# Kernel tuning notes

Measured on AMD Instinct MI355X. Metric: run time of the kernel, lower is better.

## Reference

```python
import jax, jax.numpy as jnp
import numpy as np

N, IN_DIM, LDIM = 8192, 512, 256
NEG_SLOPE = 0.01  # torch F.leaky_relu default
EPS = 1e-10


def setup_inputs() -> dict:
    key = jax.random.key(0)
    k1, k2, k3, k4 = jax.random.split(key, 4)
    x = jax.random.normal(k1, (N, IN_DIM), dtype=jnp.float32)
    adj = jax.random.uniform(k2, (N, N), dtype=jnp.float32)
    # nn.Linear(in_dim, learning_dim, bias=False) weight: [learning_dim, in_dim]
    proj_w = jax.random.normal(k3, (LDIM, IN_DIM), dtype=jnp.float32) * (1.0 / np.sqrt(IN_DIM))
    # nn.init.uniform_(learn_w, a=0, b=1)
    learn_w = jax.random.uniform(k4, (LDIM,), dtype=jnp.float32)
    return {"x": x, "adj": adj, "proj_w": proj_w, "learn_w": learn_w}


def reference(x, adj, proj_w, learn_w):
    # x_hat = projection(x): [N, LDIM]
    x_hat = x @ proj_w.T
    # cosine-distance score: sum_d w_d * (1 - xn_i[d] * xn_j[d])
    #   = sum(w) - (xn * w) @ xn.T  -- avoids the N x N x D intermediate
    xn = x_hat / jnp.linalg.norm(x_hat, axis=-1, keepdims=True)  # [N, LDIM]
    scores = jnp.sum(learn_w) - jnp.einsum('id,jd->ij', xn * learn_w, xn)  # [N, N]
    out = jax.nn.leaky_relu(scores, NEG_SLOPE)
    out = out - jnp.max(out, axis=-1, keepdims=True)
    soft_adj = adj * jnp.exp(out)
    soft_adj = soft_adj / jnp.sum(soft_adj, axis=-1, keepdims=True) + EPS
    return soft_adj
```

## Files before the change

kernel.cpp:

```cpp
#include <hip/hip_runtime.h>
#include <stdint.h>

#define NN 8192
#define KDIM 512
#define LDIM 256

typedef short bf16x8 __attribute__((ext_vector_type(8)));
typedef short short8 __attribute__((ext_vector_type(8)));
typedef float f32x4 __attribute__((ext_vector_type(4)));

__device__ __forceinline__ unsigned short f2bf(float f) {
  unsigned int u = __float_as_uint(f);
  u = (u + 0x7fffu + ((u >> 16) & 1u)) >> 16;
  return (unsigned short)u;
}
__device__ __forceinline__ float bf2f(unsigned short s) {
  return __uint_as_float(((unsigned int)s) << 16);
}

__device__ __forceinline__ void async_ld16(const unsigned short* g, unsigned short* l) {
  __builtin_amdgcn_global_load_lds(
      (const __attribute__((address_space(1))) unsigned int*)g,
      (__attribute__((address_space(3))) unsigned int*)l, 16, 0, 0);
}

__global__ __launch_bounds__(256) void cast_kernel(
    const float* __restrict__ x, const float* __restrict__ pw,
    unsigned short* __restrict__ xb, unsigned short* __restrict__ pwb) {
  int i = blockIdx.x * 256 + threadIdx.x;
  xb[i] = f2bf(x[i]);
  if (i < LDIM * KDIM) pwb[i] = f2bf(pw[i]);
}

__global__ __launch_bounds__(256) void norm_kernel(
    const float* __restrict__ xh, const float* __restrict__ w,
    unsigned short* __restrict__ Ab, unsigned short* __restrict__ Bb) {
  const int row = blockIdx.x;
  const int d = threadIdx.x;
  const float v = xh[row * LDIM + d];
  float ss = v * v;
#pragma unroll
  for (int m = 1; m < 64; m <<= 1) ss += __shfl_xor(ss, m);
  __shared__ float s4[4];
  if ((d & 63) == 0) s4[d >> 6] = ss;
  __syncthreads();
  const float tot = s4[0] + s4[1] + s4[2] + s4[3];
  const float inv = 1.0f / sqrtf(tot);
  const float xn = v * inv;
  Bb[row * LDIM + d] = f2bf(xn);
  Ab[row * LDIM + d] = f2bf(xn * w[d]);
}

template <int K, int MODE>
__global__ __launch_bounds__(256) void gemm_bt(
    const unsigned short* __restrict__ A,
    const unsigned short* __restrict__ B,
    float* __restrict__ C,
    unsigned short* __restrict__ T,
    const float* __restrict__ adj,
    float* __restrict__ rowsum,
    int ldC) {
  __shared__ unsigned short As[128 * 32];
  __shared__ unsigned short Bs[128 * 32];
  __shared__ float rs[128];

  const int tid = threadIdx.x;
  const int wave = tid >> 6;
  const int lane = tid & 63;
  const int quad = lane >> 4;
  const int l16 = lane & 15;
  const int wm = wave >> 1;
  const int wn = wave & 1;

  const size_t row0 = (size_t)blockIdx.y * 128;
  const size_t col0 = (size_t)blockIdx.x * 128;

  const int c0 = wave * 128 + lane;
  const int mA = c0 >> 2;
  const int kA = (c0 & 3) * 8;
  const unsigned short* Ag = A + (row0 + mA) * (size_t)K + kA;
  const unsigned short* Bg = B + (col0 + mA) * (size_t)K + kA;
  char* AsB = (char*)As;
  char* BsB = (char*)Bs;
  unsigned short* dA0 = (unsigned short*)(AsB + wave * 2048);
  unsigned short* dA1 = (unsigned short*)(AsB + wave * 2048 + 1024);
  unsigned short* dB0 = (unsigned short*)(BsB + wave * 2048);
  unsigned short* dB1 = (unsigned short*)(BsB + wave * 2048 + 1024);

  f32x4 acc[4][4];
#pragma unroll
  for (int i = 0; i < 4; ++i)
#pragma unroll
    for (int j = 0; j < 4; ++j) acc[i][j] = (f32x4)(0.0f);

  for (int k0 = 0; k0 < K; k0 += 32) {
    async_ld16(Ag + k0, dA0);
    async_ld16(Ag + 16 * (size_t)K + k0, dA1);
    async_ld16(Bg + k0, dB0);
    async_ld16(Bg + 16 * (size_t)K + k0, dB1);
    __syncthreads();

    bf16x8 av[4], bv[4];
#pragma unroll
    for (int mt = 0; mt < 4; ++mt)
      av[mt] = *(const bf16x8*)(AsB + (wm * 64 + mt * 16 + l16) * 64 + quad * 16);
#pragma unroll
    for (int nt = 0; nt < 4; ++nt)
      bv[nt] = *(const bf16x8*)(BsB + (wn * 64 + nt * 16 + l16) * 64 + quad * 16);
#pragma unroll
    for (int mt = 0; mt < 4; ++mt)
#pragma unroll
      for (int nt = 0; nt < 4; ++nt)
        acc[mt][nt] = __builtin_amdgcn_mfma_f32_16x16x32_bf16(av[mt], bv[nt], acc[mt][nt], 0, 0, 0);
    __syncthreads();
  }

  if constexpr (MODE == 0) {
#pragma unroll
    for (int mt = 0; mt < 4; ++mt)
#pragma unroll
      for (int nt = 0; nt < 4; ++nt)
#pragma unroll
        for (int r = 0; r < 4; ++r) {
          size_t gr = row0 + wm * 64 + mt * 16 + quad * 4 + r;
          size_t gc = col0 + wn * 64 + nt * 16 + l16;
          C[gr * (size_t)ldC + gc] = acc[mt][nt][r];
        }
  } else {
    __shared__ float trans[32 * 132];
    const int s = tid >> 3;
    const int cb = tid & 7;
    const int coff = cb * 16;
#pragma unroll
    for (int mt = 0; mt < 4; ++mt) {
      __syncthreads();
#pragma unroll
      for (int nt = 0; nt < 4; ++nt)
#pragma unroll
        for (int r = 0; r < 4; ++r)
          trans[(wm * 16 + quad * 4 + r) * 132 + wn * 64 + nt * 16 + l16] =
              acc[mt][nt][r];
      __syncthreads();
      const size_t gr = row0 + (size_t)(s >> 4) * 64 + mt * 16 + (s & 15);
      const float* arow = adj + gr * NN + col0 + coff;
      float av16[16];
#pragma unroll
      for (int q = 0; q < 4; ++q) {
        float4 a4 = ((const float4*)arow)[q];
        av16[q * 4 + 0] = a4.x;
        av16[q * 4 + 1] = a4.y;
        av16[q * 4 + 2] = a4.z;
        av16[q * 4 + 3] = a4.w;
      }
      const float* drow = &trans[s * 132 + coff];
      float part = 0.0f;
      if constexpr (MODE == 1) {
        short8 p0, p1;
#pragma unroll
        for (int j = 0; j < 16; ++j) {
          float tv = av16[j] * __expf(-drow[j]);
          unsigned short us = f2bf(tv);
          part += bf2f(us);
          if (j < 8) p0[j] = (short)us; else p1[j - 8] = (short)us;
        }
        short8* trow = (short8*)(T + gr * NN + col0 + coff);
        trow[0] = p0;
        trow[1] = p1;
      } else {
        float4 o[4];
#pragma unroll
        for (int j = 0; j < 16; ++j) {
          float tv = av16[j] * __expf(-drow[j]);
          part += tv;
          ((float*)o)[j] = tv;
        }
        float4* crow = (float4*)(C + gr * NN + col0 + coff);
#pragma unroll
        for (int q = 0; q < 4; ++q) crow[q] = o[q];
      }
      part += __shfl_xor(part, 1);
      part += __shfl_xor(part, 2);
      part += __shfl_xor(part, 4);
      if (cb == 0) rs[(s >> 4) * 64 + mt * 16 + (s & 15)] = part;
    }
    __syncthreads();
    if (tid < 128) atomicAdd(&rowsum[row0 + tid], rs[tid]);
  }
}

__global__ __launch_bounds__(256) void scale_bf16_kernel(
    const unsigned short* __restrict__ T, const float* __restrict__ rowsum,
    float* __restrict__ out) {
  const size_t i = (size_t)blockIdx.x * 256 + threadIdx.x;
  const int row = (int)(i >> 10);
  short8 tv = ((const short8*)T)[i];
  const float inv = 1.0f / rowsum[row];
  float4 o0, o1;
  o0.x = bf2f((unsigned short)tv[0]) * inv + 1e-10f;
  o0.y = bf2f((unsigned short)tv[1]) * inv + 1e-10f;
  o0.z = bf2f((unsigned short)tv[2]) * inv + 1e-10f;
  o0.w = bf2f((unsigned short)tv[3]) * inv + 1e-10f;
  o1.x = bf2f((unsigned short)tv[4]) * inv + 1e-10f;
  o1.y = bf2f((unsigned short)tv[5]) * inv + 1e-10f;
  o1.z = bf2f((unsigned short)tv[6]) * inv + 1e-10f;
  o1.w = bf2f((unsigned short)tv[7]) * inv + 1e-10f;
  ((float4*)out)[i * 2] = o0;
  ((float4*)out)[i * 2 + 1] = o1;
}

__global__ __launch_bounds__(256) void scale_f32_kernel(
    float* __restrict__ t, const float* __restrict__ rowsum) {
  const size_t i = (size_t)blockIdx.x * 256 + threadIdx.x;
  const int row = (int)(i >> 11);
  float4 v = ((float4*)t)[i];
  const float inv = 1.0f / rowsum[row];
  v.x = v.x * inv + 1e-10f;
  v.y = v.y * inv + 1e-10f;
  v.z = v.z * inv + 1e-10f;
  v.w = v.w * inv + 1e-10f;
  ((float4*)t)[i] = v;
}

extern "C" void kernel_launch(void* const* d_in, const int* in_sizes, int n_in,
                              void* d_out, int out_size, void* d_ws, size_t ws_size,
                              hipStream_t stream) {
  (void)in_sizes; (void)n_in; (void)out_size;
  const float* x   = (const float*)d_in[0];
  const float* adj = (const float*)d_in[1];
  const float* pw  = (const float*)d_in[2];
  const float* lw  = (const float*)d_in[3];
  float* out = (float*)d_out;
  char* ws = (char*)d_ws;

  unsigned short* xb   = (unsigned short*)(ws);
  unsigned short* pwb  = (unsigned short*)(ws + 8388608);
  float*          xhat = (float*)(ws + 8650752);
  unsigned short* Ab   = (unsigned short*)(ws + 17039360);
  unsigned short* Bb   = (unsigned short*)(ws + 21233664);
  float*          rsum = (float*)(ws + 25427968);
  unsigned short* Tbuf = (unsigned short*)(ws + 25460736);
  const bool big_ws = ws_size >= 25460736ull + (size_t)NN * NN * 2ull;

  cast_kernel<<<(NN * KDIM) / 256, 256, 0, stream>>>(x, pw, xb, pwb);
  gemm_bt<KDIM, 0><<<dim3(2, 64), 256, 0, stream>>>(xb, pwb, xhat, nullptr, nullptr, nullptr, LDIM);
  norm_kernel<<<NN, 256, 0, stream>>>(xhat, lw, Ab, Bb);
  hipMemsetAsync(rsum, 0, NN * sizeof(float), stream);
  if (big_ws) {
    gemm_bt<LDIM, 1><<<dim3(64, 64), 256, 0, stream>>>(Ab, Bb, nullptr, Tbuf, adj, rsum, NN);
    scale_bf16_kernel<<<(NN / 8) * (NN / 256), 256, 0, stream>>>(Tbuf, rsum, out);
  } else {
    gemm_bt<LDIM, 2><<<dim3(64, 64), 256, 0, stream>>>(Ab, Bb, out, nullptr, adj, rsum, NN);
    scale_f32_kernel<<<(NN / 4) * (NN / 256), 256, 0, stream>>>(out, rsum);
  }
}
```

Baseline: 542.9 us.

## Fuse projection GEMM with row normalization, vectorize cast, swizzle score GEMM blocks

Replaces the projection GEMM plus separate norm kernel with one kernel. Each block computes a 32-row slab across all 256 output columns, reduces the row norms from the accumulators, and writes the normalized bf16 A/B operands directly, so the fp32 x_hat round trip and one launch go away. The cast kernel now handles four elements per thread with float4 loads. The big score GEMM remaps block indices with a swizzle, meant to improve L2 reuse of the A/B tiles. The large score GEMM and its adj/output traffic still dominate, so the overall effect may be small.

```diff
diff --git a/kernel.cpp b/kernel.cpp
--- a/kernel.cpp
+++ b/kernel.cpp
@@ -8,6 +8,7 @@
 typedef short bf16x8 __attribute__((ext_vector_type(8)));
 typedef short short8 __attribute__((ext_vector_type(8)));
 typedef float f32x4 __attribute__((ext_vector_type(4)));
+typedef unsigned short u16x4 __attribute__((ext_vector_type(4)));
 
 __device__ __forceinline__ unsigned short f2bf(float f) {
   unsigned int u = __float_as_uint(f);
@@ -18,7 +19,7 @@
   return __uint_as_float(((unsigned int)s) << 16);
 }
 
-__device__ __forceinline__ void async_ld16(const unsigned short* g, unsigned short* l) {
+__device__ __forceinline__ void async_ld16(const unsigned short* g, void* l) {
   __builtin_amdgcn_global_load_lds(
       (const __attribute__((address_space(1))) unsigned int*)g,
       (__attribute__((address_space(3))) unsigned int*)l, 16, 0, 0);
@@ -27,28 +28,125 @@
 __global__ __launch_bounds__(256) void cast_kernel(
     const float* __restrict__ x, const float* __restrict__ pw,
     unsigned short* __restrict__ xb, unsigned short* __restrict__ pwb) {
-  int i = blockIdx.x * 256 + threadIdx.x;
-  xb[i] = f2bf(x[i]);
-  if (i < LDIM * KDIM) pwb[i] = f2bf(pw[i]);
-}
-
-__global__ __launch_bounds__(256) void norm_kernel(
-    const float* __restrict__ xh, const float* __restrict__ w,
+  const int i = blockIdx.x * 256 + threadIdx.x;
+  float4 v = ((const float4*)x)[i];
+  u16x4 o;
+  o[0] = (short)f2bf(v.x); o[1] = (short)f2bf(v.y);
+  o[2] = (short)f2bf(v.z); o[3] = (short)f2bf(v.w);
+  ((u16x4*)xb)[i] = o;
+  if (i < (LDIM * KDIM) / 4) {
+    float4 w = ((const float4*)pw)[i];
+    u16x4 ow;
+    ow[0] = (short)f2bf(w.x); ow[1] = (short)f2bf(w.y);
+    ow[2] = (short)f2bf(w.z); ow[3] = (short)f2bf(w.w);
+    ((u16x4*)pwb)[i] = ow;
+  }
+}
+
+__global__ __launch_bounds__(256) void gemm1_norm_kernel(
+    const unsigned short* __restrict__ xb,
+    const unsigned short* __restrict__ pwb,
+    const float* __restrict__ w,
     unsigned short* __restrict__ Ab, unsigned short* __restrict__ Bb) {
-  const int row = blockIdx.x;
-  const int d = threadIdx.x;
-  const float v = xh[row * LDIM + d];
-  float ss = v * v;
-#pragma unroll
-  for (int m = 1; m < 64; m <<= 1) ss += __shfl_xor(ss, m);
-  __shared__ float s4[4];
-  if ((d & 63) == 0) s4[d >> 6] = ss;
+  __shared__ alignas(16) unsigned short As[32 * 32];
+  __shared__ alignas(16) unsigned short Bs[256 * 32];
+  __shared__ float nrm[32][5];
+  __shared__ float wS[LDIM];
+  __shared__ alignas(16) unsigned short xnS[32][264];
+  __shared__ alignas(16) unsigned short anS[32][264];
+
+  const int tid = threadIdx.x;
+  const int wave = tid >> 6;
+  const int lane = tid & 63;
+  const int quad = lane >> 4;
+  const int l16 = lane & 15;
+  const size_t row0 = (size_t)blockIdx.x * 32;
+
+  if (tid < LDIM) wS[tid] = w[tid];
+
+  f32x4 acc[2][4];
+#pragma unroll
+  for (int i = 0; i < 2; ++i)
+#pragma unroll
+    for (int j = 0; j < 4; ++j) acc[i][j] = (f32x4)(0.0f);
+
+  for (int k0 = 0; k0 < KDIM; k0 += 32) {
+#pragma unroll
+    for (int j = 0; j < 4; ++j) {
+      const int c = (wave * 4 + j) * 64 + lane;
+      async_ld16(pwb + (size_t)(c >> 2) * KDIM + (c & 3) * 8 + k0,
+                 (char*)Bs + (wave * 4 + j) * 1024);
+    }
+    if (wave == 0) {
+#pragma unroll
+      for (int j2 = 0; j2 < 2; ++j2) {
+        const int c = j2 * 64 + lane;
+        async_ld16(xb + (row0 + (c >> 2)) * (size_t)KDIM + (c & 3) * 8 + k0,
+                   (char*)As + j2 * 1024);
+      }
+    }
+    __syncthreads();
+    bf16x8 av[2], bv[4];
+#pragma unroll
+    for (int mt = 0; mt < 2; ++mt)
+      av[mt] = *(const bf16x8*)(As + (mt * 16 + l16) * 32 + quad * 8);
+#pragma unroll
+    for (int nt = 0; nt < 4; ++nt)
+      bv[nt] = *(const bf16x8*)(Bs + (wave * 64 + nt * 16 + l16) * 32 + quad * 8);
+#pragma unroll
+    for (int mt = 0; mt < 2; ++mt)
+#pragma unroll
+      for (int nt = 0; nt < 4; ++nt)
+        acc[mt][nt] = __builtin_amdgcn_mfma_f32_16x16x32_bf16(
+            av[mt], bv[nt], acc[mt][nt], 0, 0, 0);
+    __syncthreads();
+  }
+
+#pragma unroll
+  for (int mt = 0; mt < 2; ++mt)
+#pragma unroll
+    for (int r = 0; r < 4; ++r) {
+      float s = 0.0f;
+#pragma unroll
+      for (int nt = 0; nt < 4; ++nt) s += acc[mt][nt][r] * acc[mt][nt][r];
+      s += __shfl_xor(s, 1);
+      s += __shfl_xor(s, 2);
+      s += __shfl_xor(s, 4);
+      s += __shfl_xor(s, 8);
+      if (l16 == 0) nrm[mt * 16 + quad * 4 + r][wave] = s;
+    }
   __syncthreads();
-  const float tot = s4[0] + s4[1] + s4[2] + s4[3];
-  const float inv = 1.0f / sqrtf(tot);
-  const float xn = v * inv;
-  Bb[row * LDIM + d] = f2bf(xn);
-  Ab[row * LDIM + d] = f2bf(xn * w[d]);
+  if (tid < 32)
+    nrm[tid][4] = rsqrtf(nrm[tid][0] + nrm[tid][1] + nrm[tid][2] + nrm[tid][3]);
+  __syncthreads();
+
+#pragma unroll
+  for (int mt = 0; mt < 2; ++mt)
+#pragma unroll
+    for (int r = 0; r < 4; ++r) {
+      const int row = mt * 16 + quad * 4 + r;
+      const float inv = nrm[row][4];
+#pragma unroll
+      for (int nt = 0; nt < 4; ++nt) {
+        const int col = wave * 64 + nt * 16 + l16;
+        const float xn = acc[mt][nt][r] * inv;
+        xnS[row][col] = f2bf(xn);
+        anS[row][col] = f2bf(xn * wS[col]);
+      }
+    }
+  __syncthreads();
+
+  {
+    const int row = tid >> 3;
+    const int cb = (tid & 7) * 32;
+    unsigned short* bdst = Bb + (row0 + row) * LDIM + cb;
+    unsigned short* adst = Ab + (row0 + row) * LDIM + cb;
+#pragma unroll
+    for (int q = 0; q < 4; ++q) {
+      ((short8*)bdst)[q] = *(const short8*)&xnS[row][cb + q * 8];
+      ((short8*)adst)[q] = *(const short8*)&anS[row][cb + q * 8];
+    }
+  }
 }
 
 template <int K, int MODE>
@@ -58,11 +156,11 @@
     float* __restrict__ C,
     unsigned short* __restrict__ T,
     const float* __restrict__ adj,
-    float* __restrict__ rowsum,
-    int ldC) {
+    float* __restrict__ rowsum) {
   __shared__ unsigned short As[128 * 32];
   __shared__ unsigned short Bs[128 * 32];
   __shared__ float rs[128];
+  __shared__ float trans[32 * 132];
 
   const int tid = threadIdx.x;
   const int wave = tid >> 6;
@@ -72,8 +170,10 @@
   const int wm = wave >> 1;
   const int wn = wave & 1;
 
-  const size_t row0 = (size_t)blockIdx.y * 128;
-  const size_t col0 = (size_t)blockIdx.x * 128;
+  const int lin = blockIdx.y * 64 + blockIdx.x;
+  const int swz = (lin & 7) * 512 + (lin >> 3);
+  const size_t row0 = (size_t)(swz >> 6) * 128;
+  const size_t col0 = (size_t)(swz & 63) * 128;
 
   const int c0 = wave * 128 + lane;
   const int mA = c0 >> 2;
@@ -115,77 +215,63 @@
     __syncthreads();
   }
 
-  if constexpr (MODE == 0) {
-#pragma unroll
-    for (int mt = 0; mt < 4; ++mt)
-#pragma unroll
-      for (int nt = 0; nt < 4; ++nt)
-#pragma unroll
-        for (int r = 0; r < 4; ++r) {
-          size_t gr = row0 + wm * 64 + mt * 16 + quad * 4 + r;
-          size_t gc = col0 + wn * 64 + nt * 16 + l16;
-          C[gr * (size_t)ldC + gc] = acc[mt][nt][r];
-        }
-  } else {
-    __shared__ float trans[32 * 132];
-    const int s = tid >> 3;
-    const int cb = tid & 7;
-    const int coff = cb * 16;
-#pragma unroll
-    for (int mt = 0; mt < 4; ++mt) {
-      __syncthreads();
-#pragma unroll
-      for (int nt = 0; nt < 4; ++nt)
-#pragma unroll
-        for (int r = 0; r < 4; ++r)
-          trans[(wm * 16 + quad * 4 + r) * 132 + wn * 64 + nt * 16 + l16] =
-              acc[mt][nt][r];
-      __syncthreads();
-      const size_t gr = row0 + (size_t)(s >> 4) * 64 + mt * 16 + (s & 15);
-      const float* arow = adj + gr * NN + col0 + coff;
-      float av16[16];
-#pragma unroll
-      for (int q = 0; q < 4; ++q) {
-        float4 a4 = ((const float4*)arow)[q];
-        av16[q * 4 + 0] = a4.x;
-        av16[q * 4 + 1] = a4.y;
-        av16[q * 4 + 2] = a4.z;
-        av16[q * 4 + 3] = a4.w;
+  const int s = tid >> 3;
+  const int cb = tid & 7;
+  const int coff = cb * 16;
+#pragma unroll
+  for (int mt = 0; mt < 4; ++mt) {
+    __syncthreads();
+#pragma unroll
+    for (int nt = 0; nt < 4; ++nt)
+#pragma unroll
+      for (int r = 0; r < 4; ++r)
+        trans[(wm * 16 + quad * 4 + r) * 132 + wn * 64 + nt * 16 + l16] =
+            acc[mt][nt][r];
+    __syncthreads();
+    const size_t gr = row0 + (size_t)(s >> 4) * 64 + mt * 16 + (s & 15);
+    const float* arow = adj + gr * NN + col0 + coff;
+    float av16[16];
+#pragma unroll
+    for (int q = 0; q < 4; ++q) {
+      float4 a4 = ((const float4*)arow)[q];
+      av16[q * 4 + 0] = a4.x;
+      av16[q * 4 + 1] = a4.y;
+      av16[q * 4 + 2] = a4.z;
+      av16[q * 4 + 3] = a4.w;
+    }
+    const float* drow = &trans[s * 132 + coff];
+    float part = 0.0f;
+    if constexpr (MODE == 1) {
+      short8 p0, p1;
+#pragma unroll
+      for (int j = 0; j < 16; ++j) {
+        float tv = av16[j] * __expf(-drow[j]);
+        unsigned short us = f2bf(tv);
+        part += bf2f(us);
+        if (j < 8) p0[j] = (short)us; else p1[j - 8] = (short)us;
       }
-      const float* drow = &trans[s * 132 + coff];
-      float part = 0.0f;
-      if constexpr (MODE == 1) {
-        short8 p0, p1;
-#pragma unroll
-        for (int j = 0; j < 16; ++j) {
-          float tv = av16[j] * __expf(-drow[j]);
-          unsigned short us = f2bf(tv);
-          part += bf2f(us);
-          if (j < 8) p0[j] = (short)us; else p1[j - 8] = (short)us;
-        }
-        short8* trow = (short8*)(T + gr * NN + col0 + coff);
-        trow[0] = p0;
-        trow[1] = p1;
-      } else {
-        float4 o[4];
-#pragma unroll
-        for (int j = 0; j < 16; ++j) {
-          float tv = av16[j] * __expf(-drow[j]);
-          part += tv;
-          ((float*)o)[j] = tv;
-        }
-        float4* crow = (float4*)(C + gr * NN + col0 + coff);
-#pragma unroll
-        for (int q = 0; q < 4; ++q) crow[q] = o[q];
+      short8* trow = (short8*)(T + gr * NN + col0 + coff);
+      trow[0] = p0;
+      trow[1] = p1;
+    } else {
+      float4 o[4];
+#pragma unroll
+      for (int j = 0; j < 16; ++j) {
+        float tv = av16[j] * __expf(-drow[j]);
+        part += tv;
+        ((float*)o)[j] = tv;
       }
-      part += __shfl_xor(part, 1);
-      part += __shfl_xor(part, 2);
-      part += __shfl_xor(part, 4);
-      if (cb == 0) rs[(s >> 4) * 64 + mt * 16 + (s & 15)] = part;
-    }
-    __syncthreads();
-    if (tid < 128) atomicAdd(&rowsum[row0 + tid], rs[tid]);
-  }
+      float4* crow = (float4*)(C + gr * NN + col0 + coff);
+#pragma unroll
+      for (int q = 0; q < 4; ++q) crow[q] = o[q];
+    }
+    part += __shfl_xor(part, 1);
+    part += __shfl_xor(part, 2);
+    part += __shfl_xor(part, 4);
+    if (cb == 0) rs[(s >> 4) * 64 + mt * 16 + (s & 15)] = part;
+  }
+  __syncthreads();
+  if (tid < 128) atomicAdd(&rowsum[row0 + tid], rs[tid]);
 }
 
 __global__ __launch_bounds__(256) void scale_bf16_kernel(
@@ -234,22 +320,20 @@
 
   unsigned short* xb   = (unsigned short*)(ws);
   unsigned short* pwb  = (unsigned short*)(ws + 8388608);
-  float*          xhat = (float*)(ws + 8650752);
   unsigned short* Ab   = (unsigned short*)(ws + 17039360);
   unsigned short* Bb   = (unsigned short*)(ws + 21233664);
   float*          rsum = (float*)(ws + 25427968);
   unsigned short* Tbuf = (unsigned short*)(ws + 25460736);
   const bool big_ws = ws_size >= 25460736ull + (size_t)NN * NN * 2ull;
 
-  cast_kernel<<<(NN * KDIM) / 256, 256, 0, stream>>>(x, pw, xb, pwb);
-  gemm_bt<KDIM, 0><<<dim3(2, 64), 256, 0, stream>>>(xb, pwb, xhat, nullptr, nullptr, nullptr, LDIM);
-  norm_kernel<<<NN, 256, 0, stream>>>(xhat, lw, Ab, Bb);
+  cast_kernel<<<(NN * KDIM) / (256 * 4), 256, 0, stream>>>(x, pw, xb, pwb);
+  gemm1_norm_kernel<<<NN / 32, 256, 0, stream>>>(xb, pwb, lw, Ab, Bb);
   hipMemsetAsync(rsum, 0, NN * sizeof(float), stream);
   if (big_ws) {
-    gemm_bt<LDIM, 1><<<dim3(64, 64), 256, 0, stream>>>(Ab, Bb, nullptr, Tbuf, adj, rsum, NN);
+    gemm_bt<LDIM, 1><<<dim3(64, 64), 256, 0, stream>>>(Ab, Bb, nullptr, Tbuf, adj, rsum);
     scale_bf16_kernel<<<(NN / 8) * (NN / 256), 256, 0, stream>>>(Tbuf, rsum, out);
   } else {
-    gemm_bt<LDIM, 2><<<dim3(64, 64), 256, 0, stream>>>(Ab, Bb, out, nullptr, adj, rsum, NN);
+    gemm_bt<LDIM, 2><<<dim3(64, 64), 256, 0, stream>>>(Ab, Bb, out, nullptr, adj, rsum);
     scale_f32_kernel<<<(NN / 4) * (NN / 256), 256, 0, stream>>>(out, rsum);
   }
 }
```

Result: no change. 545.5 us (+0.5%).
